# Kernel optimization log

Measured on AMD Instinct MI355X. Metric: run time of the kernel, lower is better.

Reference implementation:

```python
import jax, jax.numpy as jnp
import numpy as np

N_NODES = 100_000
N_EDGES = 3_200_000


def gcn_conv(x, edge_index, W, b, num_nodes):
    """PyG-style GCNConv: linear -> symmetric-normalized aggregation (with self-loops) -> bias."""
    xw = x @ W  # [N, out]
    # add self-loops
    loop = jnp.arange(num_nodes, dtype=edge_index.dtype)
    src = jnp.concatenate([edge_index[0], loop])
    dst = jnp.concatenate([edge_index[1], loop])
    # degree over target nodes (edge_weight = 1)
    deg = jax.ops.segment_sum(jnp.ones_like(dst, dtype=xw.dtype), dst, num_segments=num_nodes)
    dinv = jnp.where(deg > 0, jax.lax.rsqrt(deg), 0.0)
    norm = dinv[src] * dinv[dst]  # [E + N]
    msgs = norm[:, None] * xw[src]  # [E + N, out]
    out = jax.ops.segment_sum(msgs, dst, num_segments=num_nodes)
    return out + b


def setup_inputs() -> dict:
    key = jax.random.key(0)
    k1, k2, k3, k4 = jax.random.split(key, 4)
    x = jax.random.normal(k1, (N_NODES, 5), dtype=jnp.float32)
    edge_index = jax.random.randint(k2, (2, N_EDGES), 0, N_NODES, dtype=jnp.int64)
    W1 = jax.random.normal(k3, (5, 16), dtype=jnp.float32) * (1.0 / np.sqrt(5.0))
    b1 = jnp.zeros((16,), dtype=jnp.float32)
    W2 = jax.random.normal(k4, (16, 1), dtype=jnp.float32) * (1.0 / np.sqrt(16.0))
    b2 = jnp.zeros((1,), dtype=jnp.float32)
    return {"x": x, "edge_index": edge_index, "W1": W1, "b1": b1, "W2": W2, "b2": b2}


def reference(x, edge_index, W1, b1, W2, b2):
    h = jax.nn.relu(gcn_conv(x, edge_index, W1, b1, N_NODES))
    out = gcn_conv(h, edge_index, W2, b2, N_NODES)
    return out  # [N_NODES, 1]
```

## Files before the change

### kernel.cpp

```cpp
#include <hip/hip_runtime.h>

constexpr int N_NODES = 100000;
constexpr int N_EDGES = 3200000;
constexpr int F1  = 16;
constexpr int FIN = 5;
constexpr int NPB = 256;
constexpr int NB  = (N_NODES + NPB - 1) / NPB;
constexpr int TILE = 16384;
constexpr int NT  = (N_EDGES + TILE - 1) / TILE;
constexpr int TB  = 256;
constexpr int BTB = 512;

__global__ __launch_bounds__(512) void binhist_kernel(const int4* __restrict__ dst4,
                                                      int* __restrict__ tile_cnt) {
    __shared__ int lh[NB];
    int t = threadIdx.x;
    for (int b = t; b < NB; b += BTB) lh[b] = 0;
    __syncthreads();
    int base4 = blockIdx.x * (TILE / 4);
#pragma unroll
    for (int k = 0; k < TILE / (4 * BTB); ++k) {
        int i4 = base4 + k * BTB + t;
        if (i4 * 4 < N_EDGES) {
            int4 d = dst4[i4];
            atomicAdd(&lh[d.x >> 8], 1);
            atomicAdd(&lh[d.y >> 8], 1);
            atomicAdd(&lh[d.z >> 8], 1);
            atomicAdd(&lh[d.w >> 8], 1);
        }
    }
    __syncthreads();
    int* row = tile_cnt + blockIdx.x * NB;
    for (int b = t; b < NB; b += BTB) row[b] = lh[b];
}

__global__ __launch_bounds__(256) void colsum_kernel(const int* __restrict__ tile_cnt,
                                                     int* __restrict__ bin_cnt) {
    int b = blockIdx.x * TB + threadIdx.x;
    if (b >= NB) return;
    int s = 0;
    for (int i = 0; i < NT; ++i) s += tile_cnt[i * NB + b];
    bin_cnt[b] = s;
}

__global__ __launch_bounds__(512) void binscan_kernel(const int* __restrict__ bin_cnt,
                                                      int* __restrict__ bin_base) {
    __shared__ int buf[2][512];
    int t = threadIdx.x;
    int v = (t < NB) ? bin_cnt[t] : 0;
    buf[0][t] = v;
    __syncthreads();
    int cur = 0;
    for (int off = 1; off < 512; off <<= 1) {
        int nv = buf[cur][t];
        if (t >= off) nv += buf[cur][t - off];
        buf[cur ^ 1][t] = nv;
        cur ^= 1;
        __syncthreads();
    }
    if (t < NB) bin_base[t] = buf[cur][t] - v;
    if (t == 0) bin_base[NB] = N_EDGES;
}

__global__ __launch_bounds__(256) void tilebase_kernel(int* __restrict__ tile_cnt,
                                                       const int* __restrict__ bin_base) {
    int b = blockIdx.x * TB + threadIdx.x;
    if (b >= NB) return;
    int run = bin_base[b];
    for (int i = 0; i < NT; ++i) {
        int c = tile_cnt[i * NB + b];
        tile_cnt[i * NB + b] = run;
        run += c;
    }
}

__global__ __launch_bounds__(256) void repack_kernel(const float* __restrict__ x,
                                                     float* __restrict__ xpad) {
    int i = blockIdx.x * TB + threadIdx.x;
    if (i >= N_NODES) return;
#pragma unroll
    for (int k = 0; k < FIN; ++k) xpad[(size_t)i * 8 + k] = x[i * FIN + k];
}

__global__ __launch_bounds__(512) void reorder_kernel(const int4* __restrict__ src4,
                                                      const int4* __restrict__ dst4,
                                                      const int* __restrict__ tile_base,
                                                      int* __restrict__ binned) {
    __shared__ int lh[NB];
    __shared__ int lbase[NB];
    int t = threadIdx.x;
    const int* row = tile_base + blockIdx.x * NB;
    for (int b = t; b < NB; b += BTB) { lh[b] = 0; lbase[b] = row[b]; }
    __syncthreads();
    int base4 = blockIdx.x * (TILE / 4);
#pragma unroll
    for (int k = 0; k < TILE / (4 * BTB); ++k) {
        int i4 = base4 + k * BTB + t;
        if (i4 * 4 < N_EDGES) {
            int4 d = dst4[i4];
            int4 s = src4[i4];
            int b0 = d.x >> 8, b1 = d.y >> 8, b2 = d.z >> 8, b3 = d.w >> 8;
            int r0 = atomicAdd(&lh[b0], 1);
            int r1 = atomicAdd(&lh[b1], 1);
            int r2 = atomicAdd(&lh[b2], 1);
            int r3 = atomicAdd(&lh[b3], 1);
            binned[lbase[b0] + r0] = s.x | ((d.x & 255) << 24);
            binned[lbase[b1] + r1] = s.y | ((d.y & 255) << 24);
            binned[lbase[b2] + r2] = s.z | ((d.z & 255) << 24);
            binned[lbase[b3] + r3] = s.w | ((d.w & 255) << 24);
        }
    }
}

__global__ __launch_bounds__(256) void nodecsr_kernel(const int* __restrict__ binned,
                                                      const int* __restrict__ bin_base,
                                                      float* __restrict__ xpad,
                                                      int* __restrict__ node_base,
                                                      int* __restrict__ binned2) {
    __shared__ int cnt[NPB];
    __shared__ int sb[2][NPB];
    __shared__ int cur[NPB];
    int t = threadIdx.x, b = blockIdx.x;
    cnt[t] = 0;
    __syncthreads();
    int s0 = bin_base[b], s1 = bin_base[b + 1];
    int e = s0 + t;
    for (; e + 3 * TB < s1; e += 4 * TB) {
        int v0 = binned[e], v1 = binned[e + TB], v2 = binned[e + 2 * TB], v3 = binned[e + 3 * TB];
        atomicAdd(&cnt[((unsigned)v0) >> 24], 1);
        atomicAdd(&cnt[((unsigned)v1) >> 24], 1);
        atomicAdd(&cnt[((unsigned)v2) >> 24], 1);
        atomicAdd(&cnt[((unsigned)v3) >> 24], 1);
    }
    for (; e < s1; e += TB) atomicAdd(&cnt[((unsigned)binned[e]) >> 24], 1);
    __syncthreads();
    int myc = cnt[t];
    sb[0][t] = myc;
    __syncthreads();
    int c = 0;
    for (int off = 1; off < NPB; off <<= 1) {
        int nv = sb[c][t];
        if (t >= off) nv += sb[c][t - off];
        sb[c ^ 1][t] = nv;
        c ^= 1;
        __syncthreads();
    }
    int excl = sb[c][t] - myc;
    cur[t] = excl;
    int g = b * NPB + t;
    if (g < N_NODES) {
        node_base[g] = s0 + excl;
        float dv = rsqrtf((float)myc + 1.0f);
        float* row = xpad + (size_t)g * 8;
#pragma unroll
        for (int k = 0; k < FIN; ++k) row[k] *= dv;
        row[5] = dv;
    }
    if (b == NB - 1 && t == 0) node_base[N_NODES] = N_EDGES;
    __syncthreads();
    e = s0 + t;
    for (; e < s1; e += TB) {
        int v = binned[e];
        int r = atomicAdd(&cur[((unsigned)v) >> 24], 1);
        binned2[s0 + r] = v & 0x00FFFFFF;
    }
}

__global__ __launch_bounds__(256) void gather1_kernel(const int* __restrict__ binned2,
                                                      const int* __restrict__ node_base,
                                                      const float* __restrict__ xpad,
                                                      const float* __restrict__ W1,
                                                      const float* __restrict__ b1,
                                                      const float* __restrict__ W2,
                                                      float* __restrict__ zs) {
    int g = blockIdx.x * TB + threadIdx.x;
    if (g >= N_NODES) return;
    int s = node_base[g], e1 = node_base[g + 1];
    const float* own = xpad + (size_t)g * 8;
    float4 o4 = *(const float4*)own;
    float acc0 = o4.x, acc1 = o4.y, acc2 = o4.z, acc3 = o4.w, acc4 = own[4];
    float dd = own[5];
    int e = s;
    for (; e + 3 < e1; e += 4) {
        int a = binned2[e], bq = binned2[e + 1], cq = binned2[e + 2], dq = binned2[e + 3];
        const float* r0 = xpad + (size_t)a * 8;
        const float* r1 = xpad + (size_t)bq * 8;
        const float* r2 = xpad + (size_t)cq * 8;
        const float* r3 = xpad + (size_t)dq * 8;
        float4 q0 = *(const float4*)r0, q1 = *(const float4*)r1;
        float4 q2 = *(const float4*)r2, q3 = *(const float4*)r3;
        float c0 = r0[4], c1 = r1[4], c2 = r2[4], c3 = r3[4];
        acc0 += (q0.x + q1.x) + (q2.x + q3.x);
        acc1 += (q0.y + q1.y) + (q2.y + q3.y);
        acc2 += (q0.z + q1.z) + (q2.z + q3.z);
        acc3 += (q0.w + q1.w) + (q2.w + q3.w);
        acc4 += (c0 + c1) + (c2 + c3);
    }
    for (; e < e1; ++e) {
        const float* r = xpad + (size_t)binned2[e] * 8;
        float4 q = *(const float4*)r;
        acc0 += q.x; acc1 += q.y; acc2 += q.z; acc3 += q.w; acc4 += r[4];
    }
    float a0 = dd * acc0, a1 = dd * acc1, a2 = dd * acc2, a3 = dd * acc3, a4 = dd * acc4;
    float p = 0.f;
#pragma unroll
    for (int f = 0; f < F1; ++f) {
        float h = b1[f] + a0 * W1[0 * F1 + f] + a1 * W1[1 * F1 + f] + a2 * W1[2 * F1 + f]
                        + a3 * W1[3 * F1 + f] + a4 * W1[4 * F1 + f];
        p += fmaxf(h, 0.f) * W2[f];
    }
    zs[g] = dd * p;
}

__global__ __launch_bounds__(256) void gather2_kernel(const int* __restrict__ binned2,
                                                      const int* __restrict__ node_base,
                                                      const float* __restrict__ zs,
                                                      const float* __restrict__ xpad,
                                                      const float* __restrict__ b2,
                                                      float* __restrict__ out) {
    int g = blockIdx.x * TB + threadIdx.x;
    if (g >= N_NODES) return;
    int s = node_base[g], e1 = node_base[g + 1];
    float acc = zs[g];
    int e = s;
    for (; e + 3 < e1; e += 4) {
        float z0 = zs[binned2[e]], z1 = zs[binned2[e + 1]];
        float z2 = zs[binned2[e + 2]], z3 = zs[binned2[e + 3]];
        acc += (z0 + z1) + (z2 + z3);
    }
    for (; e < e1; ++e) acc += zs[binned2[e]];
    out[g] = xpad[(size_t)g * 8 + 5] * acc + b2[0];
}

extern "C" void kernel_launch(void* const* d_in, const int* in_sizes, int n_in,
                              void* d_out, int out_size, void* d_ws, size_t ws_size,
                              hipStream_t stream) {
    const float* x  = (const float*)d_in[0];
    const int*   ei = (const int*)d_in[1];
    const float* W1 = (const float*)d_in[2];
    const float* b1 = (const float*)d_in[3];
    const float* W2 = (const float*)d_in[4];
    const float* b2 = (const float*)d_in[5];
    float* out = (float*)d_out;

    float* xpad      = (float*)d_ws;
    int*   binned    = (int*)(xpad + (size_t)N_NODES * 8);
    int*   binned2   = binned + N_EDGES;
    float* zs        = (float*)(binned2 + N_EDGES);
    int*   node_base = (int*)(zs + N_NODES);
    int*   tile_cnt  = node_base + N_NODES + 1;
    int*   bin_cnt   = tile_cnt + NT * NB;
    int*   bin_base  = bin_cnt + NB;

    const int4* src4 = (const int4*)ei;
    const int4* dst4 = (const int4*)(ei + N_EDGES);

    int gB = (NB + TB - 1) / TB;
    int gN = (N_NODES + TB - 1) / TB;

    binhist_kernel<<<NT, BTB, 0, stream>>>(dst4, tile_cnt);
    colsum_kernel<<<gB, TB, 0, stream>>>(tile_cnt, bin_cnt);
    binscan_kernel<<<1, 512, 0, stream>>>(bin_cnt, bin_base);
    tilebase_kernel<<<gB, TB, 0, stream>>>(tile_cnt, bin_base);
    repack_kernel<<<gN, TB, 0, stream>>>(x, xpad);
    reorder_kernel<<<NT, BTB, 0, stream>>>(src4, dst4, tile_cnt, binned);
    nodecsr_kernel<<<NB, TB, 0, stream>>>(binned, bin_base, xpad, node_base, binned2);
    gather1_kernel<<<gN, TB, 0, stream>>>(binned2, node_base, xpad, W1, b1, W2, zs);
    gather2_kernel<<<gN, TB, 0, stream>>>(binned2, node_base, zs, xpad, b2, out);
}
```

Before: 199.7 us.

## Fuse bin scan stages, replicate LDS histograms, sort into LDS for layer-1 gather

The column-sum, bin-scan and tile-base kernels are merged into one single-block kernel, removing two launches. The per-node CSR build is split in two. A degree/scale kernel computes counts using two replicated LDS histograms to reduce atomic contention. A new sortgather kernel sorts each bin's edges into a 64KB LDS buffer, writes binned2 from there, and runs the layer-1 gather reading neighbour indices from LDS instead of global memory. The costs are a second read of the binned array, a large LDS footprint that limits occupancy, and silently dropped edges if any bin exceeds the LDS capacity.

```diff
diff --git a/kernel.cpp b/kernel.cpp
--- a/kernel.cpp
+++ b/kernel.cpp
@@ -10,67 +10,59 @@
 constexpr int NT  = (N_EDGES + TILE - 1) / TILE;
 constexpr int TB  = 256;
 constexpr int BTB = 512;
+constexpr int SCAP = 16384;
 
 __global__ __launch_bounds__(512) void binhist_kernel(const int4* __restrict__ dst4,
                                                       int* __restrict__ tile_cnt) {
-    __shared__ int lh[NB];
+    __shared__ int lh[2 * NB];
     int t = threadIdx.x;
-    for (int b = t; b < NB; b += BTB) lh[b] = 0;
-    __syncthreads();
+    for (int b = t; b < 2 * NB; b += BTB) lh[b] = 0;
+    __syncthreads();
+    int rep = ((t >> 6) & 1) * NB;
     int base4 = blockIdx.x * (TILE / 4);
 #pragma unroll
     for (int k = 0; k < TILE / (4 * BTB); ++k) {
         int i4 = base4 + k * BTB + t;
         if (i4 * 4 < N_EDGES) {
             int4 d = dst4[i4];
-            atomicAdd(&lh[d.x >> 8], 1);
-            atomicAdd(&lh[d.y >> 8], 1);
-            atomicAdd(&lh[d.z >> 8], 1);
-            atomicAdd(&lh[d.w >> 8], 1);
+            atomicAdd(&lh[rep + (d.x >> 8)], 1);
+            atomicAdd(&lh[rep + (d.y >> 8)], 1);
+            atomicAdd(&lh[rep + (d.z >> 8)], 1);
+            atomicAdd(&lh[rep + (d.w >> 8)], 1);
         }
     }
     __syncthreads();
     int* row = tile_cnt + blockIdx.x * NB;
-    for (int b = t; b < NB; b += BTB) row[b] = lh[b];
-}
-
-__global__ __launch_bounds__(256) void colsum_kernel(const int* __restrict__ tile_cnt,
-                                                     int* __restrict__ bin_cnt) {
-    int b = blockIdx.x * TB + threadIdx.x;
-    if (b >= NB) return;
-    int s = 0;
-    for (int i = 0; i < NT; ++i) s += tile_cnt[i * NB + b];
-    bin_cnt[b] = s;
-}
-
-__global__ __launch_bounds__(512) void binscan_kernel(const int* __restrict__ bin_cnt,
-                                                      int* __restrict__ bin_base) {
-    __shared__ int buf[2][512];
+    for (int b = t; b < NB; b += BTB) row[b] = lh[b] + lh[NB + b];
+}
+
+__global__ __launch_bounds__(512) void scanfuse_kernel(int* __restrict__ tile_cnt,
+                                                       int* __restrict__ bin_base) {
+    __shared__ int sb[2][512];
     int t = threadIdx.x;
-    int v = (t < NB) ? bin_cnt[t] : 0;
-    buf[0][t] = v;
+    int v = 0;
+    if (t < NB)
+        for (int i = 0; i < NT; ++i) v += tile_cnt[i * NB + t];
+    sb[0][t] = v;
     __syncthreads();
     int cur = 0;
     for (int off = 1; off < 512; off <<= 1) {
-        int nv = buf[cur][t];
-        if (t >= off) nv += buf[cur][t - off];
-        buf[cur ^ 1][t] = nv;
+        int nv = sb[cur][t];
+        if (t >= off) nv += sb[cur][t - off];
+        sb[cur ^ 1][t] = nv;
         cur ^= 1;
         __syncthreads();
     }
-    if (t < NB) bin_base[t] = buf[cur][t] - v;
+    int excl = sb[cur][t] - v;
+    if (t < NB) bin_base[t] = excl;
     if (t == 0) bin_base[NB] = N_EDGES;
-}
-
-__global__ __launch_bounds__(256) void tilebase_kernel(int* __restrict__ tile_cnt,
-                                                       const int* __restrict__ bin_base) {
-    int b = blockIdx.x * TB + threadIdx.x;
-    if (b >= NB) return;
-    int run = bin_base[b];
-    for (int i = 0; i < NT; ++i) {
-        int c = tile_cnt[i * NB + b];
-        tile_cnt[i * NB + b] = run;
-        run += c;
+    if (t < NB) {
+        int run = excl;
+        for (int i = 0; i < NT; ++i) {
+            int c = tile_cnt[i * NB + t];
+            tile_cnt[i * NB + t] = run;
+            run += c;
+        }
     }
 }
 
@@ -112,29 +104,28 @@
     }
 }
 
-__global__ __launch_bounds__(256) void nodecsr_kernel(const int* __restrict__ binned,
-                                                      const int* __restrict__ bin_base,
-                                                      float* __restrict__ xpad,
-                                                      int* __restrict__ node_base,
-                                                      int* __restrict__ binned2) {
-    __shared__ int cnt[NPB];
+__global__ __launch_bounds__(256) void degscale_kernel(const int* __restrict__ binned,
+                                                       const int* __restrict__ bin_base,
+                                                       float* __restrict__ xpad,
+                                                       int* __restrict__ node_base) {
+    __shared__ int cnt[2 * NPB];
     __shared__ int sb[2][NPB];
-    __shared__ int cur[NPB];
     int t = threadIdx.x, b = blockIdx.x;
-    cnt[t] = 0;
+    cnt[t] = 0; cnt[NPB + t] = 0;
     __syncthreads();
     int s0 = bin_base[b], s1 = bin_base[b + 1];
+    int rep = ((t >> 6) & 1) * NPB;
     int e = s0 + t;
     for (; e + 3 * TB < s1; e += 4 * TB) {
         int v0 = binned[e], v1 = binned[e + TB], v2 = binned[e + 2 * TB], v3 = binned[e + 3 * TB];
-        atomicAdd(&cnt[((unsigned)v0) >> 24], 1);
-        atomicAdd(&cnt[((unsigned)v1) >> 24], 1);
-        atomicAdd(&cnt[((unsigned)v2) >> 24], 1);
-        atomicAdd(&cnt[((unsigned)v3) >> 24], 1);
-    }
-    for (; e < s1; e += TB) atomicAdd(&cnt[((unsigned)binned[e]) >> 24], 1);
-    __syncthreads();
-    int myc = cnt[t];
+        atomicAdd(&cnt[rep + (((unsigned)v0) >> 24)], 1);
+        atomicAdd(&cnt[rep + (((unsigned)v1) >> 24)], 1);
+        atomicAdd(&cnt[rep + (((unsigned)v2) >> 24)], 1);
+        atomicAdd(&cnt[rep + (((unsigned)v3) >> 24)], 1);
+    }
+    for (; e < s1; e += TB) atomicAdd(&cnt[rep + (((unsigned)binned[e]) >> 24)], 1);
+    __syncthreads();
+    int myc = cnt[t] + cnt[NPB + t];
     sb[0][t] = myc;
     __syncthreads();
     int c = 0;
@@ -146,7 +137,6 @@
         __syncthreads();
     }
     int excl = sb[c][t] - myc;
-    cur[t] = excl;
     int g = b * NPB + t;
     if (g < N_NODES) {
         node_base[g] = s0 + excl;
@@ -157,59 +147,85 @@
         row[5] = dv;
     }
     if (b == NB - 1 && t == 0) node_base[N_NODES] = N_EDGES;
-    __syncthreads();
-    e = s0 + t;
+}
+
+__global__ __launch_bounds__(256) void sortgather_kernel(const int* __restrict__ binned,
+                                                         const int* __restrict__ bin_base,
+                                                         const int* __restrict__ node_base,
+                                                         const float* __restrict__ xpad,
+                                                         const float* __restrict__ W1,
+                                                         const float* __restrict__ b1,
+                                                         const float* __restrict__ W2,
+                                                         float* __restrict__ zs,
+                                                         int* __restrict__ binned2) {
+    __shared__ int sedge[SCAP];
+    __shared__ int st[NPB + 1];
+    __shared__ int cur[NPB];
+    int t = threadIdx.x, b = blockIdx.x;
+    int s0 = bin_base[b], s1 = bin_base[b + 1];
+    int tot = s1 - s0;
+    int g = b * NPB + t;
+    int mystart = (g < N_NODES) ? node_base[g] - s0 : tot;
+    st[t] = mystart;
+    cur[t] = mystart;
+    if (t == 0) st[NPB] = tot;
+    __syncthreads();
+    int e = s0 + t;
+    for (; e + 3 * TB < s1; e += 4 * TB) {
+        int v0 = binned[e], v1 = binned[e + TB], v2 = binned[e + 2 * TB], v3 = binned[e + 3 * TB];
+        int r0 = atomicAdd(&cur[((unsigned)v0) >> 24], 1);
+        int r1 = atomicAdd(&cur[((unsigned)v1) >> 24], 1);
+        int r2 = atomicAdd(&cur[((unsigned)v2) >> 24], 1);
+        int r3 = atomicAdd(&cur[((unsigned)v3) >> 24], 1);
+        if (r0 < SCAP) sedge[r0] = v0 & 0x00FFFFFF;
+        if (r1 < SCAP) sedge[r1] = v1 & 0x00FFFFFF;
+        if (r2 < SCAP) sedge[r2] = v2 & 0x00FFFFFF;
+        if (r3 < SCAP) sedge[r3] = v3 & 0x00FFFFFF;
+    }
     for (; e < s1; e += TB) {
         int v = binned[e];
         int r = atomicAdd(&cur[((unsigned)v) >> 24], 1);
-        binned2[s0 + r] = v & 0x00FFFFFF;
-    }
-}
-
-__global__ __launch_bounds__(256) void gather1_kernel(const int* __restrict__ binned2,
-                                                      const int* __restrict__ node_base,
-                                                      const float* __restrict__ xpad,
-                                                      const float* __restrict__ W1,
-                                                      const float* __restrict__ b1,
-                                                      const float* __restrict__ W2,
-                                                      float* __restrict__ zs) {
-    int g = blockIdx.x * TB + threadIdx.x;
-    if (g >= N_NODES) return;
-    int s = node_base[g], e1 = node_base[g + 1];
-    const float* own = xpad + (size_t)g * 8;
-    float4 o4 = *(const float4*)own;
-    float acc0 = o4.x, acc1 = o4.y, acc2 = o4.z, acc3 = o4.w, acc4 = own[4];
-    float dd = own[5];
-    int e = s;
-    for (; e + 3 < e1; e += 4) {
-        int a = binned2[e], bq = binned2[e + 1], cq = binned2[e + 2], dq = binned2[e + 3];
-        const float* r0 = xpad + (size_t)a * 8;
-        const float* r1 = xpad + (size_t)bq * 8;
-        const float* r2 = xpad + (size_t)cq * 8;
-        const float* r3 = xpad + (size_t)dq * 8;
-        float4 q0 = *(const float4*)r0, q1 = *(const float4*)r1;
-        float4 q2 = *(const float4*)r2, q3 = *(const float4*)r3;
-        float c0 = r0[4], c1 = r1[4], c2 = r2[4], c3 = r3[4];
-        acc0 += (q0.x + q1.x) + (q2.x + q3.x);
-        acc1 += (q0.y + q1.y) + (q2.y + q3.y);
-        acc2 += (q0.z + q1.z) + (q2.z + q3.z);
-        acc3 += (q0.w + q1.w) + (q2.w + q3.w);
-        acc4 += (c0 + c1) + (c2 + c3);
-    }
-    for (; e < e1; ++e) {
-        const float* r = xpad + (size_t)binned2[e] * 8;
-        float4 q = *(const float4*)r;
-        acc0 += q.x; acc1 += q.y; acc2 += q.z; acc3 += q.w; acc4 += r[4];
-    }
-    float a0 = dd * acc0, a1 = dd * acc1, a2 = dd * acc2, a3 = dd * acc3, a4 = dd * acc4;
-    float p = 0.f;
-#pragma unroll
-    for (int f = 0; f < F1; ++f) {
-        float h = b1[f] + a0 * W1[0 * F1 + f] + a1 * W1[1 * F1 + f] + a2 * W1[2 * F1 + f]
-                        + a3 * W1[3 * F1 + f] + a4 * W1[4 * F1 + f];
-        p += fmaxf(h, 0.f) * W2[f];
-    }
-    zs[g] = dd * p;
+        if (r < SCAP) sedge[r] = v & 0x00FFFFFF;
+    }
+    __syncthreads();
+    for (int i = t; i < tot; i += TB) binned2[s0 + i] = sedge[i];
+    if (g < N_NODES) {
+        int a = st[t], a1 = st[t + 1];
+        const float* own = xpad + (size_t)g * 8;
+        float4 o4 = *(const float4*)own;
+        float acc0 = o4.x, acc1 = o4.y, acc2 = o4.z, acc3 = o4.w, acc4 = own[4];
+        float dd = own[5];
+        int i = a;
+        for (; i + 3 < a1; i += 4) {
+            int n0 = sedge[i], n1 = sedge[i + 1], n2 = sedge[i + 2], n3 = sedge[i + 3];
+            const float* r0 = xpad + (size_t)n0 * 8;
+            const float* r1 = xpad + (size_t)n1 * 8;
+            const float* r2 = xpad + (size_t)n2 * 8;
+            const float* r3 = xpad + (size_t)n3 * 8;
+            float4 q0 = *(const float4*)r0, q1 = *(const float4*)r1;
+            float4 q2 = *(const float4*)r2, q3 = *(const float4*)r3;
+            float c0 = r0[4], c1 = r1[4], c2 = r2[4], c3 = r3[4];
+            acc0 += (q0.x + q1.x) + (q2.x + q3.x);
+            acc1 += (q0.y + q1.y) + (q2.y + q3.y);
+            acc2 += (q0.z + q1.z) + (q2.z + q3.z);
+            acc3 += (q0.w + q1.w) + (q2.w + q3.w);
+            acc4 += (c0 + c1) + (c2 + c3);
+        }
+        for (; i < a1; ++i) {
+            const float* r = xpad + (size_t)sedge[i] * 8;
+            float4 q = *(const float4*)r;
+            acc0 += q.x; acc1 += q.y; acc2 += q.z; acc3 += q.w; acc4 += r[4];
+        }
+        float a0 = dd * acc0, a1f = dd * acc1, a2 = dd * acc2, a3 = dd * acc3, a4 = dd * acc4;
+        float p = 0.f;
+#pragma unroll
+        for (int f = 0; f < F1; ++f) {
+            float h = b1[f] + a0 * W1[0 * F1 + f] + a1f * W1[1 * F1 + f] + a2 * W1[2 * F1 + f]
+                            + a3 * W1[3 * F1 + f] + a4 * W1[4 * F1 + f];
+            p += fmaxf(h, 0.f) * W2[f];
+        }
+        zs[g] = dd * p;
+    }
 }
 
 __global__ __launch_bounds__(256) void gather2_kernel(const int* __restrict__ binned2,
@@ -249,22 +265,19 @@
     float* zs        = (float*)(binned2 + N_EDGES);
     int*   node_base = (int*)(zs + N_NODES);
     int*   tile_cnt  = node_base + N_NODES + 1;
-    int*   bin_cnt   = tile_cnt + NT * NB;
-    int*   bin_base  = bin_cnt + NB;
+    int*   bin_base  = tile_cnt + NT * NB;
 
     const int4* src4 = (const int4*)ei;
     const int4* dst4 = (const int4*)(ei + N_EDGES);
 
-    int gB = (NB + TB - 1) / TB;
     int gN = (N_NODES + TB - 1) / TB;
 
     binhist_kernel<<<NT, BTB, 0, stream>>>(dst4, tile_cnt);
-    colsum_kernel<<<gB, TB, 0, stream>>>(tile_cnt, bin_cnt);
-    binscan_kernel<<<1, 512, 0, stream>>>(bin_cnt, bin_base);
-    tilebase_kernel<<<gB, TB, 0, stream>>>(tile_cnt, bin_base);
+    scanfuse_kernel<<<1, 512, 0, stream>>>(tile_cnt, bin_base);
     repack_kernel<<<gN, TB, 0, stream>>>(x, xpad);
     reorder_kernel<<<NT, BTB, 0, stream>>>(src4, dst4, tile_cnt, binned);
-    nodecsr_kernel<<<NB, TB, 0, stream>>>(binned, bin_base, xpad, node_base, binned2);
-    gather1_kernel<<<gN, TB, 0, stream>>>(binned2, node_base, xpad, W1, b1, W2, zs);
+    degscale_kernel<<<NB, TB, 0, stream>>>(binned, bin_base, xpad, node_base);
+    sortgather_kernel<<<NB, TB, 0, stream>>>(binned, bin_base, node_base, xpad,
+                                             W1, b1, W2, zs, binned2);
     gather2_kernel<<<gN, TB, 0, stream>>>(binned2, node_base, zs, xpad, b2, out);
 }
```

Result: faster. 178.5 us (-10.6%).
